# Optimization experiments

Hardware: AMD Instinct MI355X
Metric: run time of the kernel (lower is better)

The kernel has to match this reference:

```python
import jax, jax.numpy as jnp
import numpy as np

B_J0 = 0.01
LENS = 0.5
GAMMA = 0.5
BETA = 1.8
R_M = 1.0
DT = 1.0


@jax.custom_vjp
def act_fun_adp(x):
    return (x > 0).astype(x.dtype)

def _act_fwd(x):
    return (x > 0).astype(x.dtype), x

def _act_bwd(x, g):
    # Gaussian surrogate gradient (config.gradient_type == 'G')
    temp = jnp.exp(-x ** 2 / (2 * LENS ** 2)) / jnp.sqrt(2 * jnp.pi) / LENS
    return (g * temp * GAMMA,)

act_fun_adp.defvjp(_act_fwd, _act_bwd)


def setup_inputs() -> dict:
    key = jax.random.key(0)
    ks = jax.random.split(key, 20)
    B, T, I, H, O = 256, 250, 700, 512, 20
    inp = {}
    inp['input'] = (jax.random.uniform(ks[0], (B, T, I)) < 0.1).astype(jnp.float32)  # sparse spikes
    inp['mask'] = (jax.random.uniform(ks[1], (2, H, H)) < 0.8).astype(jnp.float32)
    inp['hid1_mem0'] = jax.random.uniform(ks[2], (B, H)) * 0.1
    inp['hid2_mem0'] = jax.random.uniform(ks[3], (B, H)) * 0.1
    inp['out_mem0'] = jax.random.uniform(ks[4], (B, O)) * 0.1
    # parameters (xavier-ish init)
    def xav(k, shape):
        lim = np.sqrt(6.0 / (shape[0] + shape[1]))
        return jax.random.uniform(k, shape, minval=-lim, maxval=lim)
    inp['W_in'] = xav(ks[5], (H, I)); inp['b_in'] = jnp.zeros((H,))
    inp['W_h11'] = 0.2 * xav(ks[6], (H, H)); inp['b_h11'] = jnp.zeros((H,))
    inp['W_h12'] = xav(ks[7], (H, H)); inp['b_h12'] = jnp.zeros((H,))
    inp['W_h22'] = 0.2 * xav(ks[8], (H, H)); inp['b_h22'] = jnp.zeros((H,))
    inp['W_out'] = xav(ks[9], (O, H)); inp['b_o'] = jnp.zeros((O,))
    inp['tau_adp_h1'] = 150.0 + 10.0 * jax.random.normal(ks[10], (H,))
    inp['tau_adp_h2'] = 150.0 + 10.0 * jax.random.normal(ks[11], (H,))
    inp['tau_m_h1'] = 20.0 + 5.0 * jax.random.normal(ks[12], (H,))
    inp['tau_m_h2'] = 20.0 + 5.0 * jax.random.normal(ks[13], (H,))
    inp['tau_m_o'] = 20.0 + 5.0 * jax.random.normal(ks[14], (O,))
    return inp


def reference(input, mask, hid1_mem0, hid2_mem0, out_mem0,
              W_in, b_in, W_h11, b_h11, W_h12, b_h12, W_h22, b_h22,
              W_out, b_o, tau_adp_h1, tau_adp_h2, tau_m_h1, tau_m_h2, tau_m_o):
    T = input.shape[1]
    # recurrent weights masked once before the time loop (weight.data *= mask.T)
    W_h11e = W_h11 * mask[0].T
    W_h22e = W_h22 * mask[1].T
    # per-neuron decay factors (constant across time)
    alpha1 = jnp.exp(-DT / tau_m_h1)
    alpha2 = jnp.exp(-DT / tau_m_h2)
    alpha_o = jnp.exp(-DT / tau_m_o)
    ro1 = jnp.exp(-DT / tau_adp_h1)
    ro2 = jnp.exp(-DT / tau_adp_h2)

    xs = jnp.transpose(input, (1, 0, 2))  # [T, B, I]

    def step(carry, x_t):
        mem1, spk1, mem2, spk2, outm, acc, s1, s2 = carry
        # layer 1 (note: b fed in is always b_j0, matching the torch code)
        b1 = ro1 * B_J0 + (1 - ro1) * spk1
        B1 = B_J0 + BETA * b1
        i1 = x_t @ W_in.T + b_in + spk1 @ W_h11e.T + b_h11
        mem1 = mem1 * alpha1 + (1 - alpha1) * R_M * i1 - B1 * spk1 * DT
        spk1 = act_fun_adp(mem1 - B1)
        # layer 2
        b2 = ro2 * B_J0 + (1 - ro2) * spk2
        B2 = B_J0 + BETA * b2
        i2 = spk1 @ W_h12.T + b_h12 + spk2 @ W_h22e.T + b_h22
        mem2 = mem2 * alpha2 + (1 - alpha2) * R_M * i2 - B2 * spk2 * DT
        spk2 = act_fun_adp(mem2 - B2)
        # leaky-integrator readout (no spike)
        io = spk2 @ W_out.T + b_o
        outm = outm * alpha_o + (1 - alpha_o) * R_M * io
        acc = acc + jax.nn.softmax(outm, axis=1)
        return (mem1, spk1, mem2, spk2, outm, acc, s1 + spk1, s2 + spk2), None

    B = input.shape[0]
    H = W_in.shape[0]
    O = W_out.shape[0]
    carry0 = (hid1_mem0, jnp.zeros((B, H)), hid2_mem0, jnp.zeros((B, H)),
              out_mem0, jnp.zeros((B, O)), jnp.zeros((B, H)), jnp.zeros((B, H)))
    carry, _ = jax.lax.scan(step, carry0, xs)
    _, _, _, _, _, output, s1, s2 = carry
    A_norm = jnp.sum(jnp.abs(W_h11e)) + jnp.sum(jnp.abs(W_h22e))
    return output, s1 / T, s2 / T, A_norm
```

## Files before the change

kernel.cpp:

```cpp
#include <hip/hip_runtime.h>

constexpr int BATCH = 256;
constexpr int TSTEPS = 250;
constexpr int NI = 700;
constexpr int NH = 512;
constexpr int NO = 20;
constexpr int NT = 768;
constexpr int NWAVE = 12;
constexpr int NSLICE = 6;

constexpr int OFF_WIN = 0;
constexpr int OFF_W11 = NI * NH;
constexpr int OFF_W12 = OFF_W11 + NH * NH;
constexpr int OFF_W22 = OFF_W12 + NH * NH;

#define B_J0  0.01f
#define BETA_ 1.8f

__global__ void transpose_mask(const float* __restrict__ in, const float* __restrict__ mask,
                               float* __restrict__ out, int R, int C) {
    __shared__ float tile[32][33];
    int cb = blockIdx.x * 32, rb = blockIdx.y * 32;
    int tx = threadIdx.x, ty = threadIdx.y;
    #pragma unroll
    for (int i = 0; i < 32; i += 8) {
        int r = rb + ty + i, c = cb + tx;
        if (r < R && c < C) tile[ty + i][tx] = in[(size_t)r * C + c];
    }
    __syncthreads();
    #pragma unroll
    for (int i = 0; i < 32; i += 8) {
        int c = cb + ty + i, r = rb + tx;
        if (c < C && r < R) {
            float v = tile[tx][ty + i];
            if (mask) v *= mask[(size_t)c * R + r];
            out[(size_t)c * R + r] = v;
        }
    }
}

__global__ void transpose_wout(const float* __restrict__ in, float* __restrict__ out) {
    int idx = blockIdx.x * blockDim.x + threadIdx.x;
    if (idx < NH * NO) {
        int j = idx / NO, o = idx % NO;
        out[idx] = in[o * NH + j];
    }
}

__global__ void anorm_stage1(const float* __restrict__ Wh11, const float* __restrict__ Wh22,
                             const float* __restrict__ mask, float* __restrict__ partial) {
    __shared__ float red[256];
    int tid = threadIdx.x;
    float s = 0.f;
    for (int idx = blockIdx.x * 256 + tid; idx < NH * NH; idx += 256 * 128) {
        int hh = idx / NH, j = idx % NH;
        s += fabsf(Wh11[idx] * mask[j * NH + hh]);
        s += fabsf(Wh22[idx] * mask[NH * NH + j * NH + hh]);
    }
    red[tid] = s;
    __syncthreads();
    for (int st = 128; st > 0; st >>= 1) {
        if (tid < st) red[tid] += red[tid + st];
        __syncthreads();
    }
    if (tid == 0) partial[blockIdx.x] = red[0];
}

__global__ void anorm_stage2(const float* __restrict__ partial, float* __restrict__ out) {
    __shared__ float red[128];
    int tid = threadIdx.x;
    red[tid] = partial[tid];
    __syncthreads();
    for (int st = 64; st > 0; st >>= 1) {
        if (tid < st) red[tid] += red[tid + st];
        __syncthreads();
    }
    if (tid == 0) out[0] = red[0];
}

__device__ __forceinline__ void f4add(float4& a, const float4 b) {
    a.x += b.x; a.y += b.y; a.z += b.z; a.w += b.w;
}

__device__ __forceinline__ float4 gather8(const int* __restrict__ list, int kb, int ke,
                                          const float* __restrict__ W, int q) {
    float4 a0{0,0,0,0}, a1{0,0,0,0}, a2{0,0,0,0}, a3{0,0,0,0},
           a4{0,0,0,0}, a5{0,0,0,0}, a6{0,0,0,0}, a7{0,0,0,0};
    int k = kb;
    const int q4 = q << 2;
    for (; k + 7 < ke; k += 8) {
        int o0 = list[k],     o1 = list[k + 1], o2 = list[k + 2], o3 = list[k + 3];
        int o4 = list[k + 4], o5 = list[k + 5], o6 = list[k + 6], o7 = list[k + 7];
        float4 v0 = *reinterpret_cast<const float4*>(W + o0 + q4);
        float4 v1 = *reinterpret_cast<const float4*>(W + o1 + q4);
        float4 v2 = *reinterpret_cast<const float4*>(W + o2 + q4);
        float4 v3 = *reinterpret_cast<const float4*>(W + o3 + q4);
        float4 v4 = *reinterpret_cast<const float4*>(W + o4 + q4);
        float4 v5 = *reinterpret_cast<const float4*>(W + o5 + q4);
        float4 v6 = *reinterpret_cast<const float4*>(W + o6 + q4);
        float4 v7 = *reinterpret_cast<const float4*>(W + o7 + q4);
        f4add(a0, v0); f4add(a1, v1); f4add(a2, v2); f4add(a3, v3);
        f4add(a4, v4); f4add(a5, v5); f4add(a6, v6); f4add(a7, v7);
    }
    for (; k < ke; ++k)
        f4add(a0, *reinterpret_cast<const float4*>(W + list[k] + q4));
    f4add(a0, a1); f4add(a2, a3); f4add(a4, a5); f4add(a6, a7);
    f4add(a0, a2); f4add(a4, a6); f4add(a0, a4);
    return a0;
}

__global__ __launch_bounds__(NT, 3) void snn_kernel(
    const float* __restrict__ input,
    const float* __restrict__ h1m0, const float* __restrict__ h2m0, const float* __restrict__ om0,
    const float* __restrict__ b_in, const float* __restrict__ b_h11,
    const float* __restrict__ b_h12, const float* __restrict__ b_h22,
    const float* __restrict__ b_o,
    const float* __restrict__ tau_adp_h1, const float* __restrict__ tau_adp_h2,
    const float* __restrict__ tau_m_h1, const float* __restrict__ tau_m_h2,
    const float* __restrict__ tau_m_o,
    const float* __restrict__ ws, const float* __restrict__ WoutT,
    float* __restrict__ out)
{
    __shared__ int actA[NH + NI];
    __shared__ int actB[2 * NH];
    __shared__ int cnt1[NWAVE], cnt2[NWAVE], cntI[NWAVE];
    __shared__ float4 part4a[NSLICE * 128];
    __shared__ float4 part4b[NSLICE * 128];
    __shared__ float part[320];

    const int tid = threadIdx.x;
    const int b = blockIdx.x;
    const int h = tid;
    const int s = tid >> 7;
    const int q = tid & 127;
    const int lane = tid & 63;
    const int w = tid >> 6;
    const unsigned long long ltmask = (1ull << lane) - 1ull;
    const bool isN = tid < NH;
    const bool isI = tid < NI;

    float mem1 = 0.f, mem2 = 0.f, spk1 = 0.f, spk2 = 0.f, s1c = 0.f, s2c = 0.f;
    float al1 = 0.f, al2 = 0.f, ro1 = 0.f, ro2 = 0.f, bs1 = 0.f, bs2 = 0.f;
    if (isN) {
        mem1 = h1m0[b * NH + h];
        mem2 = h2m0[b * NH + h];
        al1 = expf(-1.f / tau_m_h1[h]);
        al2 = expf(-1.f / tau_m_h2[h]);
        ro1 = expf(-1.f / tau_adp_h1[h]);
        ro2 = expf(-1.f / tau_adp_h2[h]);
        bs1 = b_in[h] + b_h11[h];
        bs2 = b_h12[h] + b_h22[h];
    }

    float outm = 0.f, accO = 0.f, alo = 0.f, bo = 0.f;
    if (tid < NO) {
        outm = om0[b * NO + tid];
        alo = expf(-1.f / tau_m_o[tid]);
        bo = b_o[tid];
    }

    const float* xbase = input + (size_t)b * TSTEPS * NI;

    int lenA = 0, lenB = 0, prevN1 = 0, prevN2 = 0;
    {
        float xc = isI ? __builtin_nontemporal_load(xbase + tid) : 0.f;
        unsigned long long mI = __ballot(xc > 0.f);
        if (lane == 0) cntI[w] = __popcll(mI);
        __syncthreads();
        int oI = 0, nI = 0;
        #pragma unroll
        for (int i = 0; i < NWAVE; ++i) {
            int ci = cntI[i];
            if (i < w) oI += ci;
            nI += ci;
        }
        if (xc > 0.f) actA[oI + __popcll(mI & ltmask)] = OFF_WIN + (tid << 9);
        lenA = nI;
        __syncthreads();
    }

    for (int k = 0; k <= TSTEPS + 1; ++k) {
        const bool hasNext = (k + 1) < TSTEPS;
        float xn = 0.f;
        if (hasNext && isI)
            xn = __builtin_nontemporal_load(xbase + (size_t)(k + 1) * NI + tid);

        if (k < TSTEPS) {
            float4 pa = gather8(actA, (lenA * s) / NSLICE, (lenA * (s + 1)) / NSLICE, ws, q);
            part4a[(s << 7) + q] = pa;
        }
        if (k >= 1 && k <= TSTEPS) {
            float4 pb = gather8(actB, (lenB * s) / NSLICE, (lenB * (s + 1)) / NSLICE, ws, q);
            part4b[(s << 7) + q] = pb;
        }
        if (k >= 2 && tid < 320) {
            int o = tid % NO, r = tid / NO;
            float p = 0.f;
            for (int kk = r; kk < prevN2; kk += 16) {
                int j = (actB[prevN1 + kk] - OFF_W22) >> 9;
                p += WoutT[j * NO + o];
            }
            part[tid] = p;
        }
        __syncthreads();

        const float* pfa = (const float*)part4a;
        const float* pfb = (const float*)part4b;
        float ns1 = 0.f, ns2 = 0.f;
        if (k < TSTEPS && isN) {
            float i1 = (((pfa[h] + pfa[NH + h]) + (pfa[2 * NH + h] + pfa[3 * NH + h])) +
                        (pfa[4 * NH + h] + pfa[5 * NH + h])) + bs1;
            float b1 = ro1 * B_J0 + (1.f - ro1) * spk1;
            float B1 = B_J0 + BETA_ * b1;
            mem1 = mem1 * al1 + (1.f - al1) * i1 - B1 * spk1;
            ns1 = (mem1 - B1) > 0.f ? 1.f : 0.f;
            spk1 = ns1; s1c += ns1;
        }
        if (k >= 1 && k <= TSTEPS && isN) {
            float i2 = (((pfb[h] + pfb[NH + h]) + (pfb[2 * NH + h] + pfb[3 * NH + h])) +
                        (pfb[4 * NH + h] + pfb[5 * NH + h])) + bs2;
            float b2 = ro2 * B_J0 + (1.f - ro2) * spk2;
            float B2 = B_J0 + BETA_ * b2;
            mem2 = mem2 * al2 + (1.f - al2) * i2 - B2 * spk2;
            ns2 = (mem2 - B2) > 0.f ? 1.f : 0.f;
            spk2 = ns2; s2c += ns2;
        }
        unsigned long long m1 = __ballot(ns1 != 0.f);
        unsigned long long m2 = __ballot(ns2 != 0.f);
        bool fI = hasNext && isI && (xn > 0.f);
        unsigned long long mI = __ballot(fI);
        if (lane == 0) {
            cnt1[w] = __popcll(m1); cnt2[w] = __popcll(m2); cntI[w] = __popcll(mI);
        }
        if (k >= 2 && tid < 64) {
            float io = bo, v = -__builtin_huge_valf(), e = 0.f;
            if (tid < NO) {
                #pragma unroll
                for (int r = 0; r < 16; ++r) io += part[r * NO + tid];
                outm = outm * alo + (1.f - alo) * io;
                v = outm;
            }
            float mx = v;
            #pragma unroll
            for (int off = 16; off > 0; off >>= 1) mx = fmaxf(mx, __shfl_xor(mx, off, 32));
            if (tid < NO) e = expf(outm - mx);
            float ssum = e;
            #pragma unroll
            for (int off = 16; off > 0; off >>= 1) ssum += __shfl_xor(ssum, off, 32);
            if (tid < NO) accO += e / ssum;
        }
        __syncthreads();

        int o1 = 0, n1 = 0, o2 = 0, n2 = 0, oI = 0, nI = 0;
        #pragma unroll
        for (int i = 0; i < NWAVE; ++i) {
            int c1 = cnt1[i], c2 = cnt2[i], ci = cntI[i];
            if (i < w) { o1 += c1; o2 += c2; oI += ci; }
            n1 += c1; n2 += c2; nI += ci;
        }
        if (ns1 != 0.f) {
            int p1 = o1 + __popcll(m1 & ltmask);
            actA[p1] = OFF_W11 + (h << 9);
            actB[p1] = OFF_W12 + (h << 9);
        }
        if (ns2 != 0.f)
            actB[n1 + o2 + __popcll(m2 & ltmask)] = OFF_W22 + (h << 9);
        if (fI) actA[n1 + oI + __popcll(mI & ltmask)] = OFF_WIN + (tid << 9);
        lenA = n1 + nI;
        lenB = n1 + n2;
        prevN1 = n1; prevN2 = n2;
        __syncthreads();
    }

    if (tid < NO) out[b * NO + tid] = accO;
    if (isN) {
        out[BATCH * NO + (size_t)b * NH + h] = s1c * (1.f / TSTEPS);
        out[BATCH * NO + BATCH * NH + (size_t)b * NH + h] = s2c * (1.f / TSTEPS);
    }
}

extern "C" void kernel_launch(void* const* d_in, const int* in_sizes, int n_in,
                              void* d_out, int out_size, void* d_ws, size_t ws_size,
                              hipStream_t stream) {
    const float* input      = (const float*)d_in[0];
    const float* mask       = (const float*)d_in[1];
    const float* h1m0       = (const float*)d_in[2];
    const float* h2m0       = (const float*)d_in[3];
    const float* om0        = (const float*)d_in[4];
    const float* W_in       = (const float*)d_in[5];
    const float* b_in       = (const float*)d_in[6];
    const float* W_h11      = (const float*)d_in[7];
    const float* b_h11      = (const float*)d_in[8];
    const float* W_h12      = (const float*)d_in[9];
    const float* b_h12      = (const float*)d_in[10];
    const float* W_h22      = (const float*)d_in[11];
    const float* b_h22      = (const float*)d_in[12];
    const float* W_out      = (const float*)d_in[13];
    const float* b_o        = (const float*)d_in[14];
    const float* tau_adp_h1 = (const float*)d_in[15];
    const float* tau_adp_h2 = (const float*)d_in[16];
    const float* tau_m_h1   = (const float*)d_in[17];
    const float* tau_m_h2   = (const float*)d_in[18];
    const float* tau_m_o    = (const float*)d_in[19];

    float* out = (float*)d_out;
    float* ws  = (float*)d_ws;

    float* WinT  = ws + OFF_WIN;
    float* Wh11T = ws + OFF_W11;
    float* Wh12T = ws + OFF_W12;
    float* Wh22T = ws + OFF_W22;
    float* WoutT = Wh22T + NH * NH;
    float* apart = WoutT + NH * NO;

    dim3 tb(32, 8);
    transpose_mask<<<dim3((NI + 31) / 32, (NH + 31) / 32), tb, 0, stream>>>(W_in, nullptr, WinT, NH, NI);
    transpose_mask<<<dim3(16, 16), tb, 0, stream>>>(W_h11, mask,            Wh11T, NH, NH);
    transpose_mask<<<dim3(16, 16), tb, 0, stream>>>(W_h12, nullptr,         Wh12T, NH, NH);
    transpose_mask<<<dim3(16, 16), tb, 0, stream>>>(W_h22, mask + NH * NH,  Wh22T, NH, NH);
    transpose_wout<<<(NH * NO + 255) / 256, 256, 0, stream>>>(W_out, WoutT);
    anorm_stage1<<<128, 256, 0, stream>>>(W_h11, W_h22, mask, apart);
    anorm_stage2<<<1, 128, 0, stream>>>(apart, out + BATCH * NO + 2 * BATCH * NH);

    snn_kernel<<<BATCH, NT, 0, stream>>>(input, h1m0, h2m0, om0,
        b_in, b_h11, b_h12, b_h22, b_o,
        tau_adp_h1, tau_adp_h2, tau_m_h1, tau_m_h2, tau_m_o,
        ws, WoutT, out);
}
```

Before: 1.390 ms.

## Widen block to 14 waves with 7 gather slices and packed wave counts

After: 1.436 ms. +3.3%, slower.

```diff
diff --git a/kernel.cpp b/kernel.cpp
--- a/kernel.cpp
+++ b/kernel.cpp
@@ -5,9 +5,9 @@
 constexpr int NI = 700;
 constexpr int NH = 512;
 constexpr int NO = 20;
-constexpr int NT = 768;
-constexpr int NWAVE = 12;
-constexpr int NSLICE = 6;
+constexpr int NT = 896;
+constexpr int NWAVE = 14;
+constexpr int NSLICE = 7;
 
 constexpr int OFF_WIN = 0;
 constexpr int OFF_W11 = NI * NH;
@@ -80,6 +80,23 @@
 
 __device__ __forceinline__ void f4add(float4& a, const float4 b) {
     a.x += b.x; a.y += b.y; a.z += b.z; a.w += b.w;
+}
+
+__device__ __forceinline__ void prefix14(const int* __restrict__ cnts, int w,
+                                         int& o1, int& n1, int& o2, int& n2,
+                                         int& oI, int& nI) {
+    const int4* cv = reinterpret_cast<const int4*>(cnts);
+    int4 A = cv[0], B = cv[1], C = cv[2], D = cv[3];
+    int cc[16] = {A.x, A.y, A.z, A.w, B.x, B.y, B.z, B.w,
+                  C.x, C.y, C.z, C.w, D.x, D.y, D.z, D.w};
+    o1 = n1 = o2 = n2 = oI = nI = 0;
+    #pragma unroll
+    for (int i = 0; i < NWAVE; ++i) {
+        int v = cc[i];
+        int a = v & 255, b2 = (v >> 8) & 255, c = (v >> 16) & 255;
+        if (i < w) { o1 += a; o2 += b2; oI += c; }
+        n1 += a; n2 += b2; nI += c;
+    }
 }
 
 __device__ __forceinline__ float4 gather8(const int* __restrict__ list, int kb, int ke,
@@ -109,7 +126,7 @@
     return a0;
 }
 
-__global__ __launch_bounds__(NT, 3) void snn_kernel(
+__global__ __launch_bounds__(NT, 2) void snn_kernel(
     const float* __restrict__ input,
     const float* __restrict__ h1m0, const float* __restrict__ h2m0, const float* __restrict__ om0,
     const float* __restrict__ b_in, const float* __restrict__ b_h11,
@@ -123,7 +140,7 @@
 {
     __shared__ int actA[NH + NI];
     __shared__ int actB[2 * NH];
-    __shared__ int cnt1[NWAVE], cnt2[NWAVE], cntI[NWAVE];
+    __shared__ int cnts[16];
     __shared__ float4 part4a[NSLICE * 128];
     __shared__ float4 part4b[NSLICE * 128];
     __shared__ float part[320];
@@ -165,15 +182,10 @@
     {
         float xc = isI ? __builtin_nontemporal_load(xbase + tid) : 0.f;
         unsigned long long mI = __ballot(xc > 0.f);
-        if (lane == 0) cntI[w] = __popcll(mI);
-        __syncthreads();
-        int oI = 0, nI = 0;
-        #pragma unroll
-        for (int i = 0; i < NWAVE; ++i) {
-            int ci = cntI[i];
-            if (i < w) oI += ci;
-            nI += ci;
-        }
+        if (lane == 0) cnts[w] = __popcll(mI) << 16;
+        __syncthreads();
+        int o1, n1, o2, n2, oI, nI;
+        prefix14(cnts, w, o1, n1, o2, n2, oI, nI);
         if (xc > 0.f) actA[oI + __popcll(mI & ltmask)] = OFF_WIN + (tid << 9);
         lenA = nI;
         __syncthreads();
@@ -209,7 +221,7 @@
         float ns1 = 0.f, ns2 = 0.f;
         if (k < TSTEPS && isN) {
             float i1 = (((pfa[h] + pfa[NH + h]) + (pfa[2 * NH + h] + pfa[3 * NH + h])) +
-                        (pfa[4 * NH + h] + pfa[5 * NH + h])) + bs1;
+                        ((pfa[4 * NH + h] + pfa[5 * NH + h]) + pfa[6 * NH + h])) + bs1;
             float b1 = ro1 * B_J0 + (1.f - ro1) * spk1;
             float B1 = B_J0 + BETA_ * b1;
             mem1 = mem1 * al1 + (1.f - al1) * i1 - B1 * spk1;
@@ -218,7 +230,7 @@
         }
         if (k >= 1 && k <= TSTEPS && isN) {
             float i2 = (((pfb[h] + pfb[NH + h]) + (pfb[2 * NH + h] + pfb[3 * NH + h])) +
-                        (pfb[4 * NH + h] + pfb[5 * NH + h])) + bs2;
+                        ((pfb[4 * NH + h] + pfb[5 * NH + h]) + pfb[6 * NH + h])) + bs2;
             float b2 = ro2 * B_J0 + (1.f - ro2) * spk2;
             float B2 = B_J0 + BETA_ * b2;
             mem2 = mem2 * al2 + (1.f - al2) * i2 - B2 * spk2;
@@ -229,9 +241,8 @@
         unsigned long long m2 = __ballot(ns2 != 0.f);
         bool fI = hasNext && isI && (xn > 0.f);
         unsigned long long mI = __ballot(fI);
-        if (lane == 0) {
-            cnt1[w] = __popcll(m1); cnt2[w] = __popcll(m2); cntI[w] = __popcll(mI);
-        }
+        if (lane == 0)
+            cnts[w] = __popcll(m1) | (__popcll(m2) << 8) | (__popcll(mI) << 16);
         if (k >= 2 && tid < 64) {
             float io = bo, v = -__builtin_huge_valf(), e = 0.f;
             if (tid < NO) {
@@ -251,13 +262,8 @@
         }
         __syncthreads();
 
-        int o1 = 0, n1 = 0, o2 = 0, n2 = 0, oI = 0, nI = 0;
-        #pragma unroll
-        for (int i = 0; i < NWAVE; ++i) {
-            int c1 = cnt1[i], c2 = cnt2[i], ci = cntI[i];
-            if (i < w) { o1 += c1; o2 += c2; oI += ci; }
-            n1 += c1; n2 += c2; nI += ci;
-        }
+        int o1, n1, o2, n2, oI, nI;
+        prefix14(cnts, w, o1, n1, o2, n2, oI, nI);
         if (ns1 != 0.f) {
             int p1 = o1 + __popcll(m1 & ltmask);
             actA[p1] = OFF_W11 + (h << 9);
```
